# Kernel tuning notes

Measured on AMD Instinct MI355X. Metric: run time of the kernel, lower is better.

Reference implementation:

```python
import jax, jax.numpy as jnp
import numpy as np

EPS = 1e-12

def cont_6d_to_rmat(d6):
    # d6: (..., 6) -> (..., 3, 3); standard Zhou et al. continuous 6D representation
    a1, a2 = d6[..., :3], d6[..., 3:]
    b1 = a1 / jnp.clip(jnp.linalg.norm(a1, axis=-1, keepdims=True), EPS)
    a2p = a2 - jnp.sum(b1 * a2, axis=-1, keepdims=True) * b1
    b2 = a2p / jnp.clip(jnp.linalg.norm(a2p, axis=-1, keepdims=True), EPS)
    b3 = jnp.cross(b1, b2)
    return jnp.stack([b1, b2, b3], axis=-1)  # b1,b2,b3 are columns


def setup_inputs() -> dict:
    key = jax.random.key(0)
    k1, k2, k3, k4, k5 = jax.random.split(key, 5)
    G, K, F, B = 400000, 20, 300, 8
    return {
        "motion_rots": jax.random.normal(k1, (K, F, 6), dtype=jnp.float32),
        "motion_transls": jax.random.normal(k2, (K, F, 3), dtype=jnp.float32),
        "motion_coefs": jax.random.normal(k3, (G, K), dtype=jnp.float32),
        "means": jax.random.normal(k4, (G, 3), dtype=jnp.float32),
        "ts": jax.random.randint(k5, (B,), 0, F),
    }


def reference(motion_rots, motion_transls, motion_coefs, means, ts):
    # compute_transforms
    mt = jnp.swapaxes(motion_transls[:, ts], 0, 1)          # (B, K, 3)
    mr = motion_rots[:, ts]                                  # (K, B, 6)
    coefs = jax.nn.softmax(motion_coefs, axis=-1)            # (G, K)
    transls = jnp.einsum('pk,nki->pni', coefs, mt)           # (G, B, 3)
    rots = jnp.einsum('pk,kni->pni', coefs, mr)              # (G, B, 6)
    rotmats = cont_6d_to_rmat(rots)                          # (G, B, 3, 3)
    transfms = jnp.concatenate([rotmats, transls[..., None]], axis=-1)  # (G, B, 3, 4)
    # compute_means: apply homogeneous transform to padded means
    means_h = jnp.concatenate([means, jnp.ones_like(means[:, :1])], axis=-1)  # (G, 4)
    return jnp.einsum('pnij,pj->pni', transfms, means_h)     # (G, B, 3)
```

## Files before the change

kernel.cpp:

```cpp
#include <hip/hip_runtime.h>


constexpr int KK  = 20;
constexpr int BB  = 8;
constexpr int BLK = 1024;
constexpr int GPB = 256;
constexpr int ROW = 12;

typedef __attribute__((ext_vector_type(2))) float f32x2;

__global__ void gather_tab(const float* __restrict__ motion_rots,
                           const float* __restrict__ motion_transls,
                           const int*   __restrict__ ts,
                           float* __restrict__ tab,
                           int F)
{
    const int tid = threadIdx.x;
    if (tid < BB * KK) {
        const int n = tid / KK, k = tid % KK;
        const int t = ts[n];
        const float* rp = motion_rots    + ((size_t)k * F + t) * 6;
        const float* tp = motion_transls + ((size_t)k * F + t) * 3;
        float* dst = tab + (n * KK + k) * ROW;
        #pragma unroll
        for (int i = 0; i < 6; ++i) dst[i] = rp[i];
        #pragma unroll
        for (int i = 0; i < 3; ++i) dst[6 + i] = tp[i];
        dst[9] = dst[10] = dst[11] = 0.f;
    }
}

__global__ __launch_bounds__(BLK) void motion_fwd(
    const float* __restrict__ motion_coefs,
    const float* __restrict__ means,
    const float* __restrict__ tab,
    float* __restrict__ out,
    int G)
{
    const int tid = threadIdx.x;
    const int wav  = __builtin_amdgcn_readfirstlane(tid >> 6);
    const int grp  = wav >> 2;
    const int q    = wav & 3;
    const int lane = tid & 63;
    const int p    = blockIdx.x * GPB + grp * 64 + lane;
    const int pc   = p < G ? p : G - 1;

    f32x2 w2[KK / 2];
    float invs;
    {
        const float4* crow = reinterpret_cast<const float4*>(motion_coefs + (size_t)pc * KK);
        float s = 0.f;
        #pragma unroll
        for (int u = 0; u < 5; ++u) {
            const float4 v = crow[u];
            const float e0 = __expf(v.x), e1 = __expf(v.y);
            const float e2 = __expf(v.z), e3 = __expf(v.w);
            w2[2*u+0] = (f32x2){e0, e1};
            w2[2*u+1] = (f32x2){e2, e3};
            s += (e0 + e1) + (e2 + e3);
        }
        invs = __builtin_amdgcn_rcpf(s);
    }
    const float mx0 = means[pc*3+0], mx1 = means[pc*3+1], mx2 = means[pc*3+2];

    auto do_slice = [&](int sl) {
        const float* tn = tab + (size_t)sl * KK * ROW;

        f32x2 a01 = {0.f, 0.f}, a23 = {0.f, 0.f};
        f32x2 a45 = {0.f, 0.f}, a67 = {0.f, 0.f};
        float a8 = 0.f;

        #pragma unroll
        for (int k = 0; k < KK; ++k) {
            const f32x2 t01 = *reinterpret_cast<const f32x2*>(tn + k*ROW + 0);
            const f32x2 t23 = *reinterpret_cast<const f32x2*>(tn + k*ROW + 2);
            const f32x2 t45 = *reinterpret_cast<const f32x2*>(tn + k*ROW + 4);
            const f32x2 t67 = *reinterpret_cast<const f32x2*>(tn + k*ROW + 6);
            const float t8  = tn[k*ROW + 8];
            const f32x2 wk  = ((k & 1) == 0)
                ? (f32x2){w2[k>>1].x, w2[k>>1].x}
                : (f32x2){w2[k>>1].y, w2[k>>1].y};
            a01 += wk * t01;
            a23 += wk * t23;
            a45 += wk * t45;
            a67 += wk * t67;
            a8   = fmaf(wk.x, t8, a8);
        }

        const float r0 = a01.x, r1 = a01.y, r2 = a23.x;
        const float r3 = a23.y, r4 = a45.x, r5 = a45.y;

        const float n1 = __builtin_amdgcn_sqrtf(fmaf(r0, r0, fmaf(r1, r1, r2*r2)));
        const float i1 = __builtin_amdgcn_rcpf(fmaxf(n1, 1e-12f));
        const float b10 = r0*i1, b11 = r1*i1, b12 = r2*i1;

        const float d  = fmaf(b10, r3, fmaf(b11, r4, b12*r5));
        const float q0 = fmaf(-d, b10, r3);
        const float q1 = fmaf(-d, b11, r4);
        const float q2 = fmaf(-d, b12, r5);
        const float n2 = __builtin_amdgcn_sqrtf(fmaf(q0, q0, fmaf(q1, q1, q2*q2)));
        const float i2 = __builtin_amdgcn_rcpf(fmaxf(n2, 1e-12f));
        const float b20 = q0*i2, b21 = q1*i2, b22 = q2*i2;

        const float b30 = fmaf(b11, b22, -(b12*b21));
        const float b31 = fmaf(b12, b20, -(b10*b22));
        const float b32 = fmaf(b10, b21, -(b11*b20));

        const float u0 = a67.x * invs;
        const float u1 = a67.y * invs;
        const float u2 = a8    * invs;

        const float o0 = fmaf(b10, mx0, fmaf(b20, mx1, fmaf(b30, mx2, u0)));
        const float o1 = fmaf(b11, mx0, fmaf(b21, mx1, fmaf(b31, mx2, u1)));
        const float o2 = fmaf(b12, mx0, fmaf(b22, mx1, fmaf(b32, mx2, u2)));

        if (p < G) {
            float* op = out + (size_t)p * (BB*3) + sl * 3;
            op[0] = o0; op[1] = o1; op[2] = o2;
        }
    };

    do_slice(q);
    do_slice(q + 4);
}

extern "C" void kernel_launch(void* const* d_in, const int* in_sizes, int n_in,
                              void* d_out, int out_size, void* d_ws, size_t ws_size,
                              hipStream_t stream) {
    const float* motion_rots    = (const float*)d_in[0];
    const float* motion_transls = (const float*)d_in[1];
    const float* motion_coefs   = (const float*)d_in[2];
    const float* means          = (const float*)d_in[3];
    const int*   ts             = (const int*)d_in[4];
    float* out = (float*)d_out;
    float* tab = (float*)d_ws;

    const int G = in_sizes[3] / 3;
    const int F = in_sizes[0] / (6 * KK);

    gather_tab<<<1, 192, 0, stream>>>(motion_rots, motion_transls, ts, tab, F);

    const int nblk = (G + GPB - 1) / GPB;
    motion_fwd<<<nblk, BLK, 0, stream>>>(motion_coefs, means, tab, out, G);
}
```

Before: 39.80 us.

## Give each wave four contiguous slices and store them as float4

```diff
diff --git a/kernel.cpp b/kernel.cpp
--- a/kernel.cpp
+++ b/kernel.cpp
@@ -3,8 +3,8 @@
 
 constexpr int KK  = 20;
 constexpr int BB  = 8;
-constexpr int BLK = 1024;
-constexpr int GPB = 256;
+constexpr int BLK = 256;
+constexpr int GPB = 128;
 constexpr int ROW = 12;
 
 typedef __attribute__((ext_vector_type(2))) float f32x2;
@@ -37,18 +37,19 @@
     float* __restrict__ out,
     int G)
 {
-    const int tid = threadIdx.x;
+    const int tid  = threadIdx.x;
     const int wav  = __builtin_amdgcn_readfirstlane(tid >> 6);
-    const int grp  = wav >> 2;
-    const int q    = wav & 3;
+    const int half = wav & 1;
+    const int q4   = wav >> 1;
     const int lane = tid & 63;
-    const int p    = blockIdx.x * GPB + grp * 64 + lane;
+    const int p    = blockIdx.x * GPB + half * 64 + lane;
     const int pc   = p < G ? p : G - 1;
 
     f32x2 w2[KK / 2];
     float invs;
     {
-        const float4* crow = reinterpret_cast<const float4*>(motion_coefs + (size_t)pc * KK);
+        const float4* crow =
+            reinterpret_cast<const float4*>(motion_coefs + (size_t)pc * KK);
         float s = 0.f;
         #pragma unroll
         for (int u = 0; u < 5; ++u) {
@@ -63,33 +64,9 @@
     }
     const float mx0 = means[pc*3+0], mx1 = means[pc*3+1], mx2 = means[pc*3+2];
 
-    auto do_slice = [&](int sl) {
-        const float* tn = tab + (size_t)sl * KK * ROW;
-
-        f32x2 a01 = {0.f, 0.f}, a23 = {0.f, 0.f};
-        f32x2 a45 = {0.f, 0.f}, a67 = {0.f, 0.f};
-        float a8 = 0.f;
-
-        #pragma unroll
-        for (int k = 0; k < KK; ++k) {
-            const f32x2 t01 = *reinterpret_cast<const f32x2*>(tn + k*ROW + 0);
-            const f32x2 t23 = *reinterpret_cast<const f32x2*>(tn + k*ROW + 2);
-            const f32x2 t45 = *reinterpret_cast<const f32x2*>(tn + k*ROW + 4);
-            const f32x2 t67 = *reinterpret_cast<const f32x2*>(tn + k*ROW + 6);
-            const float t8  = tn[k*ROW + 8];
-            const f32x2 wk  = ((k & 1) == 0)
-                ? (f32x2){w2[k>>1].x, w2[k>>1].x}
-                : (f32x2){w2[k>>1].y, w2[k>>1].y};
-            a01 += wk * t01;
-            a23 += wk * t23;
-            a45 += wk * t45;
-            a67 += wk * t67;
-            a8   = fmaf(wk.x, t8, a8);
-        }
-
-        const float r0 = a01.x, r1 = a01.y, r2 = a23.x;
-        const float r3 = a23.y, r4 = a45.x, r5 = a45.y;
-
+    auto finish = [&](float r0, float r1, float r2, float r3, float r4,
+                      float r5, float r6, float r7, float r8,
+                      float& O0, float& O1, float& O2) {
         const float n1 = __builtin_amdgcn_sqrtf(fmaf(r0, r0, fmaf(r1, r1, r2*r2)));
         const float i1 = __builtin_amdgcn_rcpf(fmaxf(n1, 1e-12f));
         const float b10 = r0*i1, b11 = r1*i1, b12 = r2*i1;
@@ -106,22 +83,59 @@
         const float b31 = fmaf(b12, b20, -(b10*b22));
         const float b32 = fmaf(b10, b21, -(b11*b20));
 
-        const float u0 = a67.x * invs;
-        const float u1 = a67.y * invs;
-        const float u2 = a8    * invs;
+        const float u0 = r6 * invs;
+        const float u1 = r7 * invs;
+        const float u2 = r8 * invs;
 
-        const float o0 = fmaf(b10, mx0, fmaf(b20, mx1, fmaf(b30, mx2, u0)));
-        const float o1 = fmaf(b11, mx0, fmaf(b21, mx1, fmaf(b31, mx2, u1)));
-        const float o2 = fmaf(b12, mx0, fmaf(b22, mx1, fmaf(b32, mx2, u2)));
-
-        if (p < G) {
-            float* op = out + (size_t)p * (BB*3) + sl * 3;
-            op[0] = o0; op[1] = o1; op[2] = o2;
-        }
+        O0 = fmaf(b10, mx0, fmaf(b20, mx1, fmaf(b30, mx2, u0)));
+        O1 = fmaf(b11, mx0, fmaf(b21, mx1, fmaf(b31, mx2, u1)));
+        O2 = fmaf(b12, mx0, fmaf(b22, mx1, fmaf(b32, mx2, u2)));
     };
 
-    do_slice(q);
-    do_slice(q + 4);
+    auto pair = [&](int sa, int sb,
+                    float& A0, float& A1, float& A2,
+                    float& B0, float& B1, float& B2) {
+        const float* ta = tab + (size_t)sa * KK * ROW;
+        const float* tb = tab + (size_t)sb * KK * ROW;
+
+        f32x2 xa01 = {0.f,0.f}, xa23 = {0.f,0.f}, xa45 = {0.f,0.f}, xa67 = {0.f,0.f};
+        f32x2 xb01 = {0.f,0.f}, xb23 = {0.f,0.f}, xb45 = {0.f,0.f}, xb67 = {0.f,0.f};
+        float xa8 = 0.f, xb8 = 0.f;
+
+        #pragma unroll
+        for (int k = 0; k < KK; ++k) {
+            const f32x2 wk = ((k & 1) == 0)
+                ? (f32x2){w2[k>>1].x, w2[k>>1].x}
+                : (f32x2){w2[k>>1].y, w2[k>>1].y};
+            xa01 += wk * *reinterpret_cast<const f32x2*>(ta + k*ROW + 0);
+            xa23 += wk * *reinterpret_cast<const f32x2*>(ta + k*ROW + 2);
+            xa45 += wk * *reinterpret_cast<const f32x2*>(ta + k*ROW + 4);
+            xa67 += wk * *reinterpret_cast<const f32x2*>(ta + k*ROW + 6);
+            xa8   = fmaf(wk.x, ta[k*ROW + 8], xa8);
+            xb01 += wk * *reinterpret_cast<const f32x2*>(tb + k*ROW + 0);
+            xb23 += wk * *reinterpret_cast<const f32x2*>(tb + k*ROW + 2);
+            xb45 += wk * *reinterpret_cast<const f32x2*>(tb + k*ROW + 4);
+            xb67 += wk * *reinterpret_cast<const f32x2*>(tb + k*ROW + 6);
+            xb8   = fmaf(wk.x, tb[k*ROW + 8], xb8);
+        }
+
+        finish(xa01.x, xa01.y, xa23.x, xa23.y, xa45.x, xa45.y,
+               xa67.x, xa67.y, xa8, A0, A1, A2);
+        finish(xb01.x, xb01.y, xb23.x, xb23.y, xb45.x, xb45.y,
+               xb67.x, xb67.y, xb8, B0, B1, B2);
+    };
+
+    float o0,o1,o2,o3,o4,o5,o6,o7,o8,o9,o10,o11;
+    const int s0 = q4 * 4;
+    pair(s0 + 0, s0 + 1, o0, o1, o2, o3,  o4,  o5);
+    pair(s0 + 2, s0 + 3, o6, o7, o8, o9,  o10, o11);
+
+    if (p < G) {
+        float4* op = reinterpret_cast<float4*>(out + (size_t)p * (BB*3) + q4 * 12);
+        op[0] = make_float4(o0, o1, o2,  o3);
+        op[1] = make_float4(o4, o5, o6,  o7);
+        op[2] = make_float4(o8, o9, o10, o11);
+    }
 }
 
 extern "C" void kernel_launch(void* const* d_in, const int* in_sizes, int n_in,
```

After: 34.79 us. 12.6% less time.
